# Kernel tuning notes

Hardware: AMD Instinct MI355X
Metric: run time of the kernel (lower is better)

The kernel has to match this reference:

```python
import jax, jax.numpy as jnp
import numpy as np

B, N, S = 16, 4096, 1024
D1, D2 = 128, 256          # points1 / points2 channel dims
IN_CH, OUT_CH = D1 + D2, 128
EPS_BN = 1e-5


def setup_inputs() -> dict:
    key = jax.random.key(0)
    ks = jax.random.split(key, 16)
    inp = {
        "xyz1": jax.random.normal(ks[0], (B, N, 3), jnp.float32),
        "xyz2": jax.random.normal(ks[1], (B, S, 3), jnp.float32),
        "points1": jax.random.normal(ks[2], (B, D1, N), jnp.float32),
        "points2": jax.random.normal(ks[3], (B, D2, S), jnp.float32),
        # fuse: 1x1 Conv (IN_CH -> OUT_CH) + BN + ReLU
        "fuse_w": jax.random.normal(ks[4], (OUT_CH, IN_CH), jnp.float32) * 0.05,
        "fuse_b": jnp.zeros((OUT_CH,), jnp.float32),
        "fuse_g": jnp.ones((OUT_CH,), jnp.float32),
        "fuse_be": jnp.zeros((OUT_CH,), jnp.float32),
        # extraction: 1 residual pointwise block (res_expansion=1.0)
        "w1": jax.random.normal(ks[5], (OUT_CH, OUT_CH), jnp.float32) * 0.05,
        "b1": jnp.zeros((OUT_CH,), jnp.float32),
        "g1": jnp.ones((OUT_CH,), jnp.float32),
        "be1": jnp.zeros((OUT_CH,), jnp.float32),
        "w2": jax.random.normal(ks[6], (OUT_CH, OUT_CH), jnp.float32) * 0.05,
        "b2": jnp.zeros((OUT_CH,), jnp.float32),
        "g2": jnp.ones((OUT_CH,), jnp.float32),
        "be2": jnp.zeros((OUT_CH,), jnp.float32),
    }
    return inp


def _bn(x, gamma, beta):
    # train-mode batchnorm over (batch, point) dims; x: [B, N, C]
    mu = jnp.mean(x, axis=(0, 1), keepdims=True)
    var = jnp.var(x, axis=(0, 1), keepdims=True)
    return (x - mu) * jax.lax.rsqrt(var + EPS_BN) * gamma + beta


def reference(xyz1, xyz2, points1, points2,
              fuse_w, fuse_b, fuse_g, fuse_be,
              w1, b1, g1, be1, w2, b2, g2, be2):
    # points2 -> [B, S, D2]
    p2 = jnp.transpose(points2, (0, 2, 1))
    # squared pairwise distances [B, N, S]
    d = (jnp.sum(xyz1 * xyz1, -1)[:, :, None]
         + jnp.sum(xyz2 * xyz2, -1)[:, None, :]
         - 2.0 * jnp.einsum("bnc,bsc->bns", xyz1, xyz2))
    # 3 nearest neighbors (equiv to full sort + [:, :, :3])
    neg_d3, idx = jax.lax.top_k(-d, 3)          # [B, N, 3]
    d3 = -neg_d3
    recip = 1.0 / (d3 + 1e-8)
    weight = recip / jnp.sum(recip, axis=2, keepdims=True)  # [B, N, 3]
    gathered = p2[jnp.arange(B)[:, None, None], idx]        # [B, N, 3, D2]
    interp = jnp.sum(gathered * weight[..., None], axis=2)  # [B, N, D2]
    # concat skip features: [B, N, D1+D2]
    feats = jnp.concatenate([jnp.transpose(points1, (0, 2, 1)), interp], axis=-1)
    # fuse: 1x1 conv + BN + ReLU
    x = jnp.einsum("bnc,oc->bno", feats, fuse_w) + fuse_b
    x = jax.nn.relu(_bn(x, fuse_g, fuse_be))
    # extraction: residual pointwise block
    h = jnp.einsum("bnc,oc->bno", x, w1) + b1
    h = jax.nn.relu(_bn(h, g1, be1))
    h = jnp.einsum("bnc,oc->bno", h, w2) + b2
    h = _bn(h, g2, be2)
    out = jax.nn.relu(h + x)
    return jnp.transpose(out, (0, 2, 1))  # [B, OUT_CH, N]
```

## Files before the change

### kernel.cpp

```cpp
#include <hip/hip_runtime.h>

#define BB   16
#define NN   4096
#define SS   1024
#define D1C  128
#define D2C  256
#define CIN  384
#define CO   128
#define MM   (BB*NN)

typedef __attribute__((ext_vector_type(8))) short short8;
typedef __attribute__((ext_vector_type(8))) unsigned short ushort8;
typedef __attribute__((ext_vector_type(4))) float f32x4;

__device__ __forceinline__ unsigned short f2bf(float f) {
  unsigned u = __builtin_bit_cast(unsigned, f);
  u += 0x7fffu + ((u >> 16) & 1u);
  return (unsigned short)(u >> 16);
}
__device__ __forceinline__ float bf2f(unsigned short u) {
  unsigned x = ((unsigned)u) << 16;
  return __builtin_bit_cast(float, x);
}
__device__ __forceinline__ unsigned cvt_pk(float lo, float hi) {
  unsigned r;
  asm("v_cvt_pk_bf16_f32 %0, %1, %2" : "=v"(r) : "v"(lo), "v"(hi));
  return r;
}
__device__ __forceinline__ ushort8 ld8(const unsigned short* p) {
  return *(const ushort8*)p;
}

__global__ __launch_bounds__(64) void arrange_all(
    const float* __restrict__ w0, const float* __restrict__ w1, const float* __restrict__ w2,
    uint4* __restrict__ wf0, uint4* __restrict__ wf1, uint4* __restrict__ wf2) {
  int blk = blockIdx.x;
  const float* w; uint4* wf; int K; int local;
  if (blk < 96)       { w = w0; wf = wf0; K = CIN; local = blk; }
  else if (blk < 128) { w = w1; wf = wf1; K = CO;  local = blk - 96; }
  else                { w = w2; wf = wf2; K = CO;  local = blk - 128; }
  int lane = threadIdx.x;
  int id = local * 64 + lane;
  int ob = (id >> 6) & 7;
  int kt = id >> 9;
  int o = ob * 16 + (lane & 15);
  int k = kt * 32 + (lane >> 4) * 8;
  const float* src = w + (size_t)o * K + k;
  union { unsigned short u[8]; uint4 v; } p;
  #pragma unroll
  for (int j = 0; j < 8; ++j) p.u[j] = f2bf(src[j]);
  wf[id] = p.v;
}

__global__ __launch_bounds__(256) void transp2(const float* __restrict__ p2,
                                               unsigned short* __restrict__ p2t) {
  int b  = blockIdx.x >> 6;
  int s0 = (blockIdx.x & 63) * 16;
  int c  = threadIdx.x;
  const float* src = p2 + ((size_t)b * D2C + c) * SS + s0;
  float v[16];
  #pragma unroll
  for (int k = 0; k < 4; ++k) {
    float4 x = *(const float4*)(src + k * 4);
    v[k*4+0] = x.x; v[k*4+1] = x.y; v[k*4+2] = x.z; v[k*4+3] = x.w;
  }
  unsigned short* dst = p2t + ((size_t)b * SS + s0) * D2C + c;
  #pragma unroll
  for (int s = 0; s < 16; ++s) dst[(size_t)s * D2C] = f2bf(v[s]);
}

__global__ __launch_bounds__(256) void transp1(const float* __restrict__ p1,
                                               unsigned short* __restrict__ p1t) {
  int b  = blockIdx.x >> 7;
  int n0 = (blockIdx.x & 127) * 32;
  int c  = threadIdx.x & 127;
  int nh = threadIdx.x >> 7;
  int n  = n0 + nh * 16;
  const float* src = p1 + ((size_t)b * D1C + c) * NN + n;
  float v[16];
  #pragma unroll
  for (int k = 0; k < 4; ++k) {
    float4 x = *(const float4*)(src + k * 4);
    v[k*4+0] = x.x; v[k*4+1] = x.y; v[k*4+2] = x.z; v[k*4+3] = x.w;
  }
  unsigned short* dst = p1t + ((size_t)b * NN + n) * D1C + c;
  #pragma unroll
  for (int s = 0; s < 16; ++s) dst[(size_t)s * D1C] = f2bf(v[s]);
}

#define INS(dd, ii) { if ((dd) < d2) { if ((dd) < d1) { if ((dd) < d0) { \
  d2=d1;i2=i1; d1=d0;i1=i0; d0=(dd);i0=(ii); } else { d2=d1;i2=i1; d1=(dd);i1=(ii); } } \
  else { d2=(dd);i2=(ii); } } }

__global__ __launch_bounds__(256) void top3_kernel(const float* __restrict__ xyz1,
                                                   const float* __restrict__ xyz2,
                                                   int* __restrict__ idx3,
                                                   float* __restrict__ w3) {
  __shared__ float4 sp[8 * 129 - 1];
  int b  = blockIdx.x >> 7;
  int nb = (blockIdx.x & 127) * 32;
  int t  = threadIdx.x;
  const float* x2 = xyz2 + (size_t)b * SS * 3;
  for (int i = t; i < SS; i += 256) {
    float a = x2[i*3+0], c = x2[i*3+1], d = x2[i*3+2];
    sp[(i >> 7) * 129 + (i & 127)] = make_float4(-2.f*a, -2.f*c, -2.f*d, a*a + c*c + d*d);
  }
  __syncthreads();
  int nl = t >> 3, q = t & 7;
  int n  = nb + nl;
  size_t gm = (size_t)b * NN + n;
  float px = xyz1[gm*3+0], py = xyz1[gm*3+1], pz = xyz1[gm*3+2];
  float d0 = 3.4e38f, d1 = 3.4e38f, d2 = 3.4e38f;
  int   i0 = 0, i1 = 0, i2 = 0;
  const float4* myq = sp + q * 129;
  int ibase = q * 128;
  #pragma unroll 4
  for (int s = 0; s < 128; ++s) {
    float4 p = myq[s];
    float d = fmaf(px, p.x, fmaf(py, p.y, fmaf(pz, p.z, p.w)));
    int i = ibase + s;
    bool c0 = d < d0, c1 = d < d1, c2 = d < d2;
    i2 = c2 ? (c1 ? i1 : i) : i2;
    i1 = c1 ? (c0 ? i0 : i) : i1;
    i0 = c0 ? i : i0;
    d2 = __builtin_amdgcn_fmed3f(d1, d2, d);
    d1 = __builtin_amdgcn_fmed3f(d0, d1, d);
    d0 = fminf(d0, d);
  }
  #pragma unroll
  for (int msk = 1; msk <= 4; msk <<= 1) {
    float e0 = __shfl_xor(d0, msk), e1 = __shfl_xor(d1, msk), e2 = __shfl_xor(d2, msk);
    int   j0 = __shfl_xor(i0, msk), j1 = __shfl_xor(i1, msk), j2 = __shfl_xor(i2, msk);
    INS(e0, j0); INS(e1, j1); INS(e2, j2);
  }
  if (q == 0) {
    float n1 = px*px + py*py + pz*pz;
    float r0 = 1.0f/(d0 + n1 + 1e-8f), r1 = 1.0f/(d1 + n1 + 1e-8f), r2 = 1.0f/(d2 + n1 + 1e-8f);
    float inv = 1.0f/(r0 + r1 + r2);
    idx3[gm*3+0] = i0; idx3[gm*3+1] = i1; idx3[gm*3+2] = i2;
    w3  [gm*3+0] = r0*inv; w3[gm*3+1] = r1*inv; w3[gm*3+2] = r2*inv;
  }
}

__device__ __forceinline__ void gemm_epilogue(
    f32x4 acc[8], const float* __restrict__ bias,
    unsigned short* __restrict__ outb, float* __restrict__ pblk,
    int m0b, int wid, int cl, int g, int t, int rawblk) {
  __shared__ unsigned short tile[64][136];
  __shared__ float sS[256], sQ[256];
  #pragma unroll
  for (int ob = 0; ob < 8; ++ob) {
    float4 bs = *(const float4*)(bias + ob * 16 + g * 4);
    float v0 = acc[ob][0] + bs.x, v1 = acc[ob][1] + bs.y;
    float v2 = acc[ob][2] + bs.z, v3 = acc[ob][3] + bs.w;
    uint2 pk;
    pk.x = cvt_pk(v0, v1);
    pk.y = cvt_pk(v2, v3);
    *(uint2*)&tile[wid * 16 + cl][ob * 16 + g * 4] = pk;
  }
  __syncthreads();
  int c = t & 127, half = t >> 7;
  float s = 0.f, q = 0.f;
  #pragma unroll
  for (int i = 0; i < 32; ++i) {
    float v = bf2f(tile[half * 32 + i][c]);
    s += v; q = fmaf(v, v, q);
  }
  sS[t] = s; sQ[t] = q;
  int m_l = t >> 2, cq = (t & 3) * 32;
  unsigned short* gdst = outb + (size_t)(m0b + m_l) * CO + cq;
  #pragma unroll
  for (int qd = 0; qd < 4; ++qd)
    *(uint4*)(gdst + qd * 8) = *(const uint4*)&tile[m_l][cq + qd * 8];
  __syncthreads();
  if (t < 128) {
    pblk[(size_t)rawblk * 256 + t]       = sS[t] + sS[t + 128];
    pblk[(size_t)rawblk * 256 + 128 + t] = sQ[t] + sQ[t + 128];
  }
}

__global__ __launch_bounds__(256, 4) void gemm1_mfma(
    const unsigned short* __restrict__ p1t, const unsigned short* __restrict__ p2t,
    const int* __restrict__ idx3, const float* __restrict__ w3,
    const uint4* __restrict__ wfrag, const float* __restrict__ bias,
    unsigned short* __restrict__ outb, float* __restrict__ pblk) {
  int t = threadIdx.x;
  int wid = t >> 6, lane = t & 63;
  int rawblk = blockIdx.x;
  int bid = (rawblk & 7) * 128 + (rawblk >> 3);
  int m0b = bid * 64;
  int m0 = m0b + wid * 16;
  int b  = m0 >> 12;
  int cl = lane & 15, g = lane >> 4;
  int m  = m0 + cl;
  int i0 = idx3[(size_t)m*3+0], i1 = idx3[(size_t)m*3+1], i2 = idx3[(size_t)m*3+2];
  float wA = w3[(size_t)m*3+0], wB = w3[(size_t)m*3+1], wC = w3[(size_t)m*3+2];
  const unsigned short* r0 = p2t + ((size_t)b * SS + i0) * D2C + g * 8;
  const unsigned short* r1 = p2t + ((size_t)b * SS + i1) * D2C + g * 8;
  const unsigned short* r2 = p2t + ((size_t)b * SS + i2) * D2C + g * 8;
  const unsigned short* pr = p1t + (size_t)m * D1C + g * 8;

  ushort8 pt[4], ua[4][3];
  #pragma unroll
  for (int kt = 0; kt < 4; ++kt) pt[kt] = ld8(pr + kt * 32);
  #pragma unroll
  for (int q = 0; q < 4; ++q) {
    int c0 = q * 32;
    ua[q][0] = ld8(r0 + c0); ua[q][1] = ld8(r1 + c0); ua[q][2] = ld8(r2 + c0);
  }
  f32x4 acc[8] = {};
  #pragma unroll
  for (int kt = 0; kt < 4; ++kt) {
    short8 bv = __builtin_bit_cast(short8, pt[kt]);
    const uint4* wk = wfrag + (size_t)kt * 512 + lane;
    #pragma unroll
    for (int ob = 0; ob < 8; ++ob)
      acc[ob] = __builtin_amdgcn_mfma_f32_16x16x32_bf16(
          __builtin_bit_cast(short8, wk[ob * 64]), bv, acc[ob], 0, 0, 0);
  }
  #pragma unroll
  for (int q = 0; q < 4; ++q) {
    float f[8];
    #pragma unroll
    for (int j = 0; j < 8; ++j)
      f[j] = wA*bf2f(ua[q][0][j]) + wB*bf2f(ua[q][1][j]) + wC*bf2f(ua[q][2][j]);
    uint4 pk;
    pk.x = cvt_pk(f[0], f[1]); pk.y = cvt_pk(f[2], f[3]);
    pk.z = cvt_pk(f[4], f[5]); pk.w = cvt_pk(f[6], f[7]);
    short8 bv = __builtin_bit_cast(short8, pk);
    const uint4* wk = wfrag + (size_t)(4 + q) * 512 + lane;
    #pragma unroll
    for (int ob = 0; ob < 8; ++ob)
      acc[ob] = __builtin_amdgcn_mfma_f32_16x16x32_bf16(
          __builtin_bit_cast(short8, wk[ob * 64]), bv, acc[ob], 0, 0, 0);
  }
  __builtin_amdgcn_sched_barrier(0);
  ushort8 ub[4][3];
  #pragma unroll
  for (int q = 0; q < 4; ++q) {
    int c0 = 128 + q * 32;
    ub[q][0] = ld8(r0 + c0); ub[q][1] = ld8(r1 + c0); ub[q][2] = ld8(r2 + c0);
  }
  #pragma unroll
  for (int q = 0; q < 4; ++q) {
    float f[8];
    #pragma unroll
    for (int j = 0; j < 8; ++j)
      f[j] = wA*bf2f(ub[q][0][j]) + wB*bf2f(ub[q][1][j]) + wC*bf2f(ub[q][2][j]);
    uint4 pk;
    pk.x = cvt_pk(f[0], f[1]); pk.y = cvt_pk(f[2], f[3]);
    pk.z = cvt_pk(f[4], f[5]); pk.w = cvt_pk(f[6], f[7]);
    short8 bv = __builtin_bit_cast(short8, pk);
    const uint4* wk = wfrag + (size_t)(8 + q) * 512 + lane;
    #pragma unroll
    for (int ob = 0; ob < 8; ++ob)
      acc[ob] = __builtin_amdgcn_mfma_f32_16x16x32_bf16(
          __builtin_bit_cast(short8, wk[ob * 64]), bv, acc[ob], 0, 0, 0);
  }
  gemm_epilogue(acc, bias, outb, pblk, m0b, wid, cl, g, t, rawblk);
}

__global__ __launch_bounds__(256, 4) void gemm23_mfma(
    const unsigned short* __restrict__ inb, const float* __restrict__ scale,
    const float* __restrict__ shift, const uint4* __restrict__ wfrag,
    const float* __restrict__ bias, unsigned short* __restrict__ outb,
    float* __restrict__ pblk) {
  int t = threadIdx.x;
  int wid = t >> 6, lane = t & 63;
  int rawblk = blockIdx.x;
  int bid = (rawblk & 7) * 128 + (rawblk >> 3);
  int m0b = bid * 64;
  int m0 = m0b + wid * 16;
  int cl = lane & 15, g = lane >> 4;
  int m  = m0 + cl;
  const unsigned short* src = inb + (size_t)m * CO + g * 8;
  ushort8 xv[4];
  #pragma unroll
  for (int kt = 0; kt < 4; ++kt) xv[kt] = ld8(src + kt * 32);
  f32x4 acc[8] = {};
  #pragma unroll
  for (int kt = 0; kt < 4; ++kt) {
    int kb = kt * 32 + g * 8;
    float4 sa = *(const float4*)(scale + kb), sb = *(const float4*)(scale + kb + 4);
    float4 ha = *(const float4*)(shift + kb), hb = *(const float4*)(shift + kb + 4);
    float f[8];
    f[0] = fmaxf(fmaf(bf2f(xv[kt][0]), sa.x, ha.x), 0.f);
    f[1] = fmaxf(fmaf(bf2f(xv[kt][1]), sa.y, ha.y), 0.f);
    f[2] = fmaxf(fmaf(bf2f(xv[kt][2]), sa.z, ha.z), 0.f);
    f[3] = fmaxf(fmaf(bf2f(xv[kt][3]), sa.w, ha.w), 0.f);
    f[4] = fmaxf(fmaf(bf2f(xv[kt][4]), sb.x, hb.x), 0.f);
    f[5] = fmaxf(fmaf(bf2f(xv[kt][5]), sb.y, hb.y), 0.f);
    f[6] = fmaxf(fmaf(bf2f(xv[kt][6]), sb.z, hb.z), 0.f);
    f[7] = fmaxf(fmaf(bf2f(xv[kt][7]), sb.w, hb.w), 0.f);
    uint4 pk;
    pk.x = cvt_pk(f[0], f[1]); pk.y = cvt_pk(f[2], f[3]);
    pk.z = cvt_pk(f[4], f[5]); pk.w = cvt_pk(f[6], f[7]);
    short8 bv = __builtin_bit_cast(short8, pk);
    const uint4* wk = wfrag + (size_t)kt * 512 + lane;
    #pragma unroll
    for (int ob = 0; ob < 8; ++ob)
      acc[ob] = __builtin_amdgcn_mfma_f32_16x16x32_bf16(
          __builtin_bit_cast(short8, wk[ob * 64]), bv, acc[ob], 0, 0, 0);
  }
  gemm_epilogue(acc, bias, outb, pblk, m0b, wid, cl, g, t, rawblk);
}

__global__ __launch_bounds__(256) void reduce_fin(const float* __restrict__ pblk,
                                                  const float* __restrict__ g,
                                                  const float* __restrict__ be,
                                                  float* __restrict__ scale,
                                                  float* __restrict__ shift) {
  int o = blockIdx.x, t = threadIdx.x;
  float s = 0.f, q = 0.f;
  #pragma unroll
  for (int it = 0; it < 4; ++it) {
    const float* p = pblk + (size_t)(it * 256 + t) * 256;
    s += p[o]; q += p[128 + o];
  }
  #pragma unroll
  for (int off = 32; off; off >>= 1) { s += __shfl_down(s, off, 64); q += __shfl_down(q, off, 64); }
  __shared__ float ls[4], lq[4];
  if ((t & 63) == 0) { ls[t >> 6] = s; lq[t >> 6] = q; }
  __syncthreads();
  if (t == 0) {
    float S = ls[0]+ls[1]+ls[2]+ls[3], Q = lq[0]+lq[1]+lq[2]+lq[3];
    const float invM = 1.0f / (float)MM;
    float mean = S * invM;
    float var  = Q * invM - mean * mean;
    float rstd = rsqrtf(var + 1e-5f);
    float sc   = g[o] * rstd;
    scale[o] = sc;
    shift[o] = fmaf(-mean, sc, be[o]);
  }
}

__global__ __launch_bounds__(256) void final_kernel(
    const unsigned short* __restrict__ bufX, const unsigned short* __restrict__ bufH2,
    const float* __restrict__ bnp, float* __restrict__ out) {
  __shared__ float yt[128][33];
  __shared__ float sb[512];
  int t = threadIdx.x;
  if (t < 128) {
    sb[t]       = bnp[t];
    sb[128 + t] = bnp[128 + t];
    sb[256 + t] = bnp[512 + t];
    sb[384 + t] = bnp[640 + t];
  }
  __syncthreads();
  int m0 = blockIdx.x * 32;
  int b  = m0 >> 12;
  int n0 = m0 & (NN - 1);
  int m_l = t >> 3;
  int cq  = (t & 7) * 16;
  size_t base = (size_t)(m0 + m_l) * CO + cq;
  ushort8 xu0 = ld8(bufX  + base), xu1 = ld8(bufX  + base + 8);
  ushort8 hu0 = ld8(bufH2 + base), hu1 = ld8(bufH2 + base + 8);
  #pragma unroll
  for (int j = 0; j < 16; ++j) {
    int c = cq + j;
    float x = bf2f(j < 8 ? xu0[j & 7] : xu1[j & 7]);
    float h = bf2f(j < 8 ? hu0[j & 7] : hu1[j & 7]);
    float y = fmaxf(fmaf(h, sb[256 + c], sb[384 + c]) +
                    fmaxf(fmaf(x, sb[c], sb[128 + c]), 0.f), 0.f);
    yt[c][m_l] = y;
  }
  __syncthreads();
  int o  = t >> 1;
  int nh = (t & 1) * 16;
  float* dst = out + (size_t)b * CO * NN + (size_t)o * NN + n0 + nh;
  #pragma unroll
  for (int qd = 0; qd < 4; ++qd)
    *(float4*)(dst + qd * 4) = make_float4(yt[o][nh + qd*4 + 0], yt[o][nh + qd*4 + 1],
                                           yt[o][nh + qd*4 + 2], yt[o][nh + qd*4 + 3]);
}

extern "C" void kernel_launch(void* const* d_in, const int* in_sizes, int n_in,
                              void* d_out, int out_size, void* d_ws, size_t ws_size,
                              hipStream_t stream) {
  const float* xyz1    = (const float*)d_in[0];
  const float* xyz2    = (const float*)d_in[1];
  const float* points1 = (const float*)d_in[2];
  const float* points2 = (const float*)d_in[3];
  const float* fuse_w  = (const float*)d_in[4];
  const float* fuse_b  = (const float*)d_in[5];
  const float* fuse_g  = (const float*)d_in[6];
  const float* fuse_be = (const float*)d_in[7];
  const float* w1      = (const float*)d_in[8];
  const float* b1      = (const float*)d_in[9];
  const float* g1      = (const float*)d_in[10];
  const float* be1     = (const float*)d_in[11];
  const float* w2      = (const float*)d_in[12];
  const float* b2      = (const float*)d_in[13];
  const float* g2      = (const float*)d_in[14];
  const float* be2     = (const float*)d_in[15];

  char* ws = (char*)d_ws;
  size_t off = 0;
  auto alloc = [&](size_t bytes) -> void* {
    void* p = ws + off;
    off += (bytes + 255) & ~(size_t)255;
    return p;
  };
  int*            idx3 = (int*)           alloc((size_t)MM * 3 * 4);
  float*          w3   = (float*)         alloc((size_t)MM * 3 * 4);
  uint4*          wf0  = (uint4*)         alloc((size_t)96 * 64 * 16);
  uint4*          wf1  = (uint4*)         alloc((size_t)32 * 64 * 16);
  uint4*          wf2  = (uint4*)         alloc((size_t)32 * 64 * 16);
  float*          pblk = (float*)         alloc((size_t)1024 * 256 * 4);
  float*          bnp  = (float*)         alloc(6 * 128 * 4);
  unsigned short* p2t  = (unsigned short*)alloc((size_t)BB * SS * D2C * 2);
  unsigned short* p1t  = (unsigned short*)alloc((size_t)MM * D1C * 2);
  unsigned short* bufX = (unsigned short*)alloc((size_t)MM * CO * 2);
  unsigned short* bufH = (unsigned short*)alloc((size_t)MM * CO * 2);
  unsigned short* bufH2= (unsigned short*)alloc((size_t)MM * CO * 2);
  if (off > ws_size) return;

  arrange_all<<<160, 64, 0, stream>>>(fuse_w, w1, w2, wf0, wf1, wf2);
  transp2<<<BB * 64, 256, 0, stream>>>(points2, p2t);
  transp1<<<BB * 128, 256, 0, stream>>>(points1, p1t);
  top3_kernel<<<MM/32, 256, 0, stream>>>(xyz1, xyz2, idx3, w3);

  gemm1_mfma<<<MM/64, 256, 0, stream>>>(p1t, p2t, idx3, w3, wf0, fuse_b, bufX, pblk);
  reduce_fin<<<128, 256, 0, stream>>>(pblk, fuse_g, fuse_be, bnp + 0, bnp + 128);

  gemm23_mfma<<<MM/64, 256, 0, stream>>>(bufX, bnp + 0, bnp + 128, wf1, b1, bufH, pblk);
  reduce_fin<<<128, 256, 0, stream>>>(pblk, g1, be1, bnp + 256, bnp + 384);

  gemm23_mfma<<<MM/64, 256, 0, stream>>>(bufH, bnp + 256, bnp + 384, wf2, b2, bufH2, pblk);
  reduce_fin<<<128, 256, 0, stream>>>(pblk, g2, be2, bnp + 512, bnp + 640);

  final_kernel<<<MM/32, 256, 0, stream>>>(bufX, bufH2, bnp, (float*)d_out);
}
```

Before: 263.9 us.

## Merge preprocessing kernels and fold BN stat reduction into GEMM epilogues

```diff
diff --git a/kernel.cpp b/kernel.cpp
--- a/kernel.cpp
+++ b/kernel.cpp
@@ -31,131 +31,137 @@
   return *(const ushort8*)p;
 }
 
-__global__ __launch_bounds__(64) void arrange_all(
-    const float* __restrict__ w0, const float* __restrict__ w1, const float* __restrict__ w2,
-    uint4* __restrict__ wf0, uint4* __restrict__ wf1, uint4* __restrict__ wf2) {
-  int blk = blockIdx.x;
-  const float* w; uint4* wf; int K; int local;
-  if (blk < 96)       { w = w0; wf = wf0; K = CIN; local = blk; }
-  else if (blk < 128) { w = w1; wf = wf1; K = CO;  local = blk - 96; }
-  else                { w = w2; wf = wf2; K = CO;  local = blk - 128; }
-  int lane = threadIdx.x;
-  int id = local * 64 + lane;
-  int ob = (id >> 6) & 7;
-  int kt = id >> 9;
-  int o = ob * 16 + (lane & 15);
-  int k = kt * 32 + (lane >> 4) * 8;
-  const float* src = w + (size_t)o * K + k;
-  union { unsigned short u[8]; uint4 v; } p;
-  #pragma unroll
-  for (int j = 0; j < 8; ++j) p.u[j] = f2bf(src[j]);
-  wf[id] = p.v;
-}
-
-__global__ __launch_bounds__(256) void transp2(const float* __restrict__ p2,
-                                               unsigned short* __restrict__ p2t) {
-  int b  = blockIdx.x >> 6;
-  int s0 = (blockIdx.x & 63) * 16;
-  int c  = threadIdx.x;
-  const float* src = p2 + ((size_t)b * D2C + c) * SS + s0;
-  float v[16];
-  #pragma unroll
-  for (int k = 0; k < 4; ++k) {
-    float4 x = *(const float4*)(src + k * 4);
-    v[k*4+0] = x.x; v[k*4+1] = x.y; v[k*4+2] = x.z; v[k*4+3] = x.w;
-  }
-  unsigned short* dst = p2t + ((size_t)b * SS + s0) * D2C + c;
-  #pragma unroll
-  for (int s = 0; s < 16; ++s) dst[(size_t)s * D2C] = f2bf(v[s]);
-}
-
-__global__ __launch_bounds__(256) void transp1(const float* __restrict__ p1,
-                                               unsigned short* __restrict__ p1t) {
-  int b  = blockIdx.x >> 7;
-  int n0 = (blockIdx.x & 127) * 32;
-  int c  = threadIdx.x & 127;
-  int nh = threadIdx.x >> 7;
-  int n  = n0 + nh * 16;
-  const float* src = p1 + ((size_t)b * D1C + c) * NN + n;
-  float v[16];
-  #pragma unroll
-  for (int k = 0; k < 4; ++k) {
-    float4 x = *(const float4*)(src + k * 4);
-    v[k*4+0] = x.x; v[k*4+1] = x.y; v[k*4+2] = x.z; v[k*4+3] = x.w;
-  }
-  unsigned short* dst = p1t + ((size_t)b * NN + n) * D1C + c;
-  #pragma unroll
-  for (int s = 0; s < 16; ++s) dst[(size_t)s * D1C] = f2bf(v[s]);
-}
-
 #define INS(dd, ii) { if ((dd) < d2) { if ((dd) < d1) { if ((dd) < d0) { \
   d2=d1;i2=i1; d1=d0;i1=i0; d0=(dd);i0=(ii); } else { d2=d1;i2=i1; d1=(dd);i1=(ii); } } \
   else { d2=(dd);i2=(ii); } } }
 
-__global__ __launch_bounds__(256) void top3_kernel(const float* __restrict__ xyz1,
-                                                   const float* __restrict__ xyz2,
-                                                   int* __restrict__ idx3,
-                                                   float* __restrict__ w3) {
-  __shared__ float4 sp[8 * 129 - 1];
-  int b  = blockIdx.x >> 7;
-  int nb = (blockIdx.x & 127) * 32;
-  int t  = threadIdx.x;
-  const float* x2 = xyz2 + (size_t)b * SS * 3;
-  for (int i = t; i < SS; i += 256) {
-    float a = x2[i*3+0], c = x2[i*3+1], d = x2[i*3+2];
-    sp[(i >> 7) * 129 + (i & 127)] = make_float4(-2.f*a, -2.f*c, -2.f*d, a*a + c*c + d*d);
-  }
-  __syncthreads();
-  int nl = t >> 3, q = t & 7;
-  int n  = nb + nl;
-  size_t gm = (size_t)b * NN + n;
-  float px = xyz1[gm*3+0], py = xyz1[gm*3+1], pz = xyz1[gm*3+2];
-  float d0 = 3.4e38f, d1 = 3.4e38f, d2 = 3.4e38f;
-  int   i0 = 0, i1 = 0, i2 = 0;
-  const float4* myq = sp + q * 129;
-  int ibase = q * 128;
-  #pragma unroll 4
-  for (int s = 0; s < 128; ++s) {
-    float4 p = myq[s];
-    float d = fmaf(px, p.x, fmaf(py, p.y, fmaf(pz, p.z, p.w)));
-    int i = ibase + s;
-    bool c0 = d < d0, c1 = d < d1, c2 = d < d2;
-    i2 = c2 ? (c1 ? i1 : i) : i2;
-    i1 = c1 ? (c0 ? i0 : i) : i1;
-    i0 = c0 ? i : i0;
-    d2 = __builtin_amdgcn_fmed3f(d1, d2, d);
-    d1 = __builtin_amdgcn_fmed3f(d0, d1, d);
-    d0 = fminf(d0, d);
-  }
-  #pragma unroll
-  for (int msk = 1; msk <= 4; msk <<= 1) {
-    float e0 = __shfl_xor(d0, msk), e1 = __shfl_xor(d1, msk), e2 = __shfl_xor(d2, msk);
-    int   j0 = __shfl_xor(i0, msk), j1 = __shfl_xor(i1, msk), j2 = __shfl_xor(i2, msk);
-    INS(e0, j0); INS(e1, j1); INS(e2, j2);
-  }
-  if (q == 0) {
-    float n1 = px*px + py*py + pz*pz;
-    float r0 = 1.0f/(d0 + n1 + 1e-8f), r1 = 1.0f/(d1 + n1 + 1e-8f), r2 = 1.0f/(d2 + n1 + 1e-8f);
-    float inv = 1.0f/(r0 + r1 + r2);
-    idx3[gm*3+0] = i0; idx3[gm*3+1] = i1; idx3[gm*3+2] = i2;
-    w3  [gm*3+0] = r0*inv; w3[gm*3+1] = r1*inv; w3[gm*3+2] = r2*inv;
+__global__ __launch_bounds__(256) void prep_kernel(
+    const float* __restrict__ xyz1, const float* __restrict__ xyz2,
+    const float* __restrict__ p1, const float* __restrict__ p2,
+    const float* __restrict__ fw, const float* __restrict__ w1, const float* __restrict__ w2,
+    int* __restrict__ idx3, float* __restrict__ w3,
+    uint4* __restrict__ wf0, uint4* __restrict__ wf1, uint4* __restrict__ wf2,
+    unsigned short* __restrict__ p2t, unsigned short* __restrict__ p1t,
+    float* __restrict__ zeroRegion) {
+  __shared__ float4 sp[1032];
+  int blk = blockIdx.x, t = threadIdx.x;
+  if (blk == 0) {
+    for (int i = t; i < 832; i += 256) zeroRegion[i] = 0.f;
+  }
+  {
+    int u = blk * 2;
+    int b = u >> 7;
+    const float* x2 = xyz2 + (size_t)b * SS * 3;
+    for (int i = t; i < SS; i += 256) {
+      float a = x2[i*3+0], c = x2[i*3+1], d = x2[i*3+2];
+      sp[(i >> 7) * 129 + (i & 127)] = make_float4(-2.f*a, -2.f*c, -2.f*d, a*a + c*c + d*d);
+    }
+    __syncthreads();
+    int nl = t >> 3, q = t & 7;
+    const float4* myq = sp + q * 129;
+    int ibase = q * 128;
+    for (int uu = 0; uu < 2; ++uu) {
+      int nb = ((u + uu) & 127) * 32;
+      int n  = nb + nl;
+      size_t gm = (size_t)b * NN + n;
+      float px = xyz1[gm*3+0], py = xyz1[gm*3+1], pz = xyz1[gm*3+2];
+      float d0 = 3.4e38f, d1 = 3.4e38f, d2 = 3.4e38f;
+      int   i0 = 0, i1 = 0, i2 = 0;
+      #pragma unroll 4
+      for (int s = 0; s < 128; ++s) {
+        float4 p = myq[s];
+        float d = fmaf(px, p.x, fmaf(py, p.y, fmaf(pz, p.z, p.w)));
+        int i = ibase + s;
+        bool c0 = d < d0, c1 = d < d1, c2 = d < d2;
+        i2 = c2 ? (c1 ? i1 : i) : i2;
+        i1 = c1 ? (c0 ? i0 : i) : i1;
+        i0 = c0 ? i : i0;
+        d2 = __builtin_amdgcn_fmed3f(d1, d2, d);
+        d1 = __builtin_amdgcn_fmed3f(d0, d1, d);
+        d0 = fminf(d0, d);
+      }
+      #pragma unroll
+      for (int msk = 1; msk <= 4; msk <<= 1) {
+        float e0 = __shfl_xor(d0, msk), e1 = __shfl_xor(d1, msk), e2 = __shfl_xor(d2, msk);
+        int   j0 = __shfl_xor(i0, msk), j1 = __shfl_xor(i1, msk), j2 = __shfl_xor(i2, msk);
+        INS(e0, j0); INS(e1, j1); INS(e2, j2);
+      }
+      if (q == 0) {
+        float n1 = px*px + py*py + pz*pz;
+        float r0 = 1.0f/(d0 + n1 + 1e-8f), r1 = 1.0f/(d1 + n1 + 1e-8f), r2 = 1.0f/(d2 + n1 + 1e-8f);
+        float inv = 1.0f/(r0 + r1 + r2);
+        idx3[gm*3+0] = i0; idx3[gm*3+1] = i1; idx3[gm*3+2] = i2;
+        w3  [gm*3+0] = r0*inv; w3[gm*3+1] = r1*inv; w3[gm*3+2] = r2*inv;
+      }
+    }
+  }
+  {
+    int b  = blk >> 6;
+    int s0 = (blk & 63) * 16;
+    int c  = t;
+    const float* src = p2 + ((size_t)b * D2C + c) * SS + s0;
+    float v[16];
+    #pragma unroll
+    for (int k = 0; k < 4; ++k) {
+      float4 x = *(const float4*)(src + k * 4);
+      v[k*4+0] = x.x; v[k*4+1] = x.y; v[k*4+2] = x.z; v[k*4+3] = x.w;
+    }
+    unsigned short* dst = p2t + ((size_t)b * SS + s0) * D2C + c;
+    #pragma unroll
+    for (int s = 0; s < 16; ++s) dst[(size_t)s * D2C] = f2bf(v[s]);
+  }
+  for (int uu = 0; uu < 2; ++uu) {
+    int u  = blk * 2 + uu;
+    int b  = u >> 7;
+    int n0 = (u & 127) * 32;
+    int c  = t & 127;
+    int n  = n0 + (t >> 7) * 16;
+    const float* src = p1 + ((size_t)b * D1C + c) * NN + n;
+    float v[16];
+    #pragma unroll
+    for (int k = 0; k < 4; ++k) {
+      float4 x = *(const float4*)(src + k * 4);
+      v[k*4+0] = x.x; v[k*4+1] = x.y; v[k*4+2] = x.z; v[k*4+3] = x.w;
+    }
+    unsigned short* dst = p1t + ((size_t)b * NN + n) * D1C + c;
+    #pragma unroll
+    for (int s = 0; s < 16; ++s) dst[(size_t)s * D1C] = f2bf(v[s]);
+  }
+  if (blk < 40) {
+    int gid = blk * 256 + t;
+    int oblk = gid >> 6, lane = gid & 63;
+    const float* w; uint4* wf; int K; int local;
+    if (oblk < 96)       { w = fw; wf = wf0; K = CIN; local = oblk; }
+    else if (oblk < 128) { w = w1; wf = wf1; K = CO;  local = oblk - 96; }
+    else                 { w = w2; wf = wf2; K = CO;  local = oblk - 128; }
+    int id = local * 64 + lane;
+    int ob = (id >> 6) & 7;
+    int kt = id >> 9;
+    int o = ob * 16 + (lane & 15);
+    int k = kt * 32 + (lane >> 4) * 8;
+    const float* src = w + (size_t)o * K + k;
+    union { unsigned short us[8]; uint4 v; } pk;
+    #pragma unroll
+    for (int j = 0; j < 8; ++j) pk.us[j] = f2bf(src[j]);
+    wf[id] = pk.v;
   }
 }
 
 __device__ __forceinline__ void gemm_epilogue(
     f32x4 acc[8], const float* __restrict__ bias,
-    unsigned short* __restrict__ outb, float* __restrict__ pblk,
-    int m0b, int wid, int cl, int g, int t, int rawblk) {
+    unsigned short* __restrict__ outb, int m0b, int wid, int cl, int g, int t,
+    float* __restrict__ gsum, float* __restrict__ gssq, unsigned* __restrict__ counter,
+    const float* __restrict__ gamma, const float* __restrict__ beta,
+    float* __restrict__ scale, float* __restrict__ shift) {
   __shared__ unsigned short tile[64][136];
   __shared__ float sS[256], sQ[256];
+  __shared__ int lastFlag;
   #pragma unroll
   for (int ob = 0; ob < 8; ++ob) {
     float4 bs = *(const float4*)(bias + ob * 16 + g * 4);
-    float v0 = acc[ob][0] + bs.x, v1 = acc[ob][1] + bs.y;
-    float v2 = acc[ob][2] + bs.z, v3 = acc[ob][3] + bs.w;
     uint2 pk;
-    pk.x = cvt_pk(v0, v1);
-    pk.y = cvt_pk(v2, v3);
+    pk.x = cvt_pk(acc[ob][0] + bs.x, acc[ob][1] + bs.y);
+    pk.y = cvt_pk(acc[ob][2] + bs.z, acc[ob][3] + bs.w);
     *(uint2*)&tile[wid * 16 + cl][ob * 16 + g * 4] = pk;
   }
   __syncthreads();
@@ -174,8 +180,24 @@
     *(uint4*)(gdst + qd * 8) = *(const uint4*)&tile[m_l][cq + qd * 8];
   __syncthreads();
   if (t < 128) {
-    pblk[(size_t)rawblk * 256 + t]       = sS[t] + sS[t + 128];
-    pblk[(size_t)rawblk * 256 + 128 + t] = sQ[t] + sQ[t + 128];
+    atomicAdd(&gsum[t], sS[t] + sS[t + 128]);
+    atomicAdd(&gssq[t], sQ[t] + sQ[t + 128]);
+  }
+  __threadfence();
+  __syncthreads();
+  if (t == 0) lastFlag = (atomicAdd(counter, 1u) == 1023u);
+  __syncthreads();
+  if (lastFlag && t < 128) {
+    __threadfence();
+    float S = atomicAdd(&gsum[t], 0.f);
+    float Q = atomicAdd(&gssq[t], 0.f);
+    const float invM = 1.0f / (float)MM;
+    float mean = S * invM;
+    float var  = Q * invM - mean * mean;
+    float rstd = rsqrtf(var + 1e-5f);
+    float sc   = gamma[t] * rstd;
+    scale[t] = sc;
+    shift[t] = fmaf(-mean, sc, beta[t]);
   }
 }
 
@@ -183,7 +205,10 @@
     const unsigned short* __restrict__ p1t, const unsigned short* __restrict__ p2t,
     const int* __restrict__ idx3, const float* __restrict__ w3,
     const uint4* __restrict__ wfrag, const float* __restrict__ bias,
-    unsigned short* __restrict__ outb, float* __restrict__ pblk) {
+    unsigned short* __restrict__ outb,
+    float* __restrict__ gsum, float* __restrict__ gssq, unsigned* __restrict__ counter,
+    const float* __restrict__ gamma, const float* __restrict__ beta,
+    float* __restrict__ scale, float* __restrict__ shift) {
   int t = threadIdx.x;
   int wid = t >> 6, lane = t & 63;
   int rawblk = blockIdx.x;
@@ -199,7 +224,6 @@
   const unsigned short* r1 = p2t + ((size_t)b * SS + i1) * D2C + g * 8;
   const unsigned short* r2 = p2t + ((size_t)b * SS + i2) * D2C + g * 8;
   const unsigned short* pr = p1t + (size_t)m * D1C + g * 8;
-
   ushort8 pt[4], ua[4][3];
   #pragma unroll
   for (int kt = 0; kt < 4; ++kt) pt[kt] = ld8(pr + kt * 32);
@@ -257,14 +281,17 @@
       acc[ob] = __builtin_amdgcn_mfma_f32_16x16x32_bf16(
           __builtin_bit_cast(short8, wk[ob * 64]), bv, acc[ob], 0, 0, 0);
   }
-  gemm_epilogue(acc, bias, outb, pblk, m0b, wid, cl, g, t, rawblk);
+  gemm_epilogue(acc, bias, outb, m0b, wid, cl, g, t,
+                gsum, gssq, counter, gamma, beta, scale, shift);
 }
 
 __global__ __launch_bounds__(256, 4) void gemm23_mfma(
-    const unsigned short* __restrict__ inb, const float* __restrict__ scale,
-    const float* __restrict__ shift, const uint4* __restrict__ wfrag,
+    const unsigned short* __restrict__ inb, const float* __restrict__ scIn,
+    const float* __restrict__ shIn, const uint4* __restrict__ wfrag,
     const float* __restrict__ bias, unsigned short* __restrict__ outb,
-    float* __restrict__ pblk) {
+    float* __restrict__ gsum, float* __restrict__ gssq, unsigned* __restrict__ counter,
+    const float* __restrict__ gamma, const float* __restrict__ beta,
+    float* __restrict__ scale, float* __restrict__ shift) {
   int t = threadIdx.x;
   int wid = t >> 6, lane = t & 63;
   int rawblk = blockIdx.x;
@@ -281,8 +308,8 @@
   #pragma unroll
   for (int kt = 0; kt < 4; ++kt) {
     int kb = kt * 32 + g * 8;
-    float4 sa = *(const float4*)(scale + kb), sb = *(const float4*)(scale + kb + 4);
-    float4 ha = *(const float4*)(shift + kb), hb = *(const float4*)(shift + kb + 4);
+    float4 sa = *(const float4*)(scIn + kb), sb = *(const float4*)(scIn + kb + 4);
+    float4 ha = *(const float4*)(shIn + kb), hb = *(const float4*)(shIn + kb + 4);
     float f[8];
     f[0] = fmaxf(fmaf(bf2f(xv[kt][0]), sa.x, ha.x), 0.f);
     f[1] = fmaxf(fmaf(bf2f(xv[kt][1]), sa.y, ha.y), 0.f);
@@ -302,36 +329,8 @@
       acc[ob] = __builtin_amdgcn_mfma_f32_16x16x32_bf16(
           __builtin_bit_cast(short8, wk[ob * 64]), bv, acc[ob], 0, 0, 0);
   }
-  gemm_epilogue(acc, bias, outb, pblk, m0b, wid, cl, g, t, rawblk);
-}
-
-__global__ __launch_bounds__(256) void reduce_fin(const float* __restrict__ pblk,
-                                                  const float* __restrict__ g,
-                                                  const float* __restrict__ be,
-                                                  float* __restrict__ scale,
-                                                  float* __restrict__ shift) {
-  int o = blockIdx.x, t = threadIdx.x;
-  float s = 0.f, q = 0.f;
-  #pragma unroll
-  for (int it = 0; it < 4; ++it) {
-    const float* p = pblk + (size_t)(it * 256 + t) * 256;
-    s += p[o]; q += p[128 + o];
-  }
-  #pragma unroll
-  for (int off = 32; off; off >>= 1) { s += __shfl_down(s, off, 64); q += __shfl_down(q, off, 64); }
-  __shared__ float ls[4], lq[4];
-  if ((t & 63) == 0) { ls[t >> 6] = s; lq[t >> 6] = q; }
-  __syncthreads();
-  if (t == 0) {
-    float S = ls[0]+ls[1]+ls[2]+ls[3], Q = lq[0]+lq[1]+lq[2]+lq[3];
-    const float invM = 1.0f / (float)MM;
-    float mean = S * invM;
-    float var  = Q * invM - mean * mean;
-    float rstd = rsqrtf(var + 1e-5f);
-    float sc   = g[o] * rstd;
-    scale[o] = sc;
-    shift[o] = fmaf(-mean, sc, be[o]);
-  }
+  gemm_epilogue(acc, bias, outb, m0b, wid, cl, g, t,
+                gsum, gssq, counter, gamma, beta, scale, shift);
 }
 
 __global__ __launch_bounds__(256) void final_kernel(
@@ -360,9 +359,8 @@
     int c = cq + j;
     float x = bf2f(j < 8 ? xu0[j & 7] : xu1[j & 7]);
     float h = bf2f(j < 8 ? hu0[j & 7] : hu1[j & 7]);
-    float y = fmaxf(fmaf(h, sb[256 + c], sb[384 + c]) +
-                    fmaxf(fmaf(x, sb[c], sb[128 + c]), 0.f), 0.f);
-    yt[c][m_l] = y;
+    yt[c][m_l] = fmaxf(fmaf(h, sb[256 + c], sb[384 + c]) +
+                       fmaxf(fmaf(x, sb[c], sb[128 + c]), 0.f), 0.f);
   }
   __syncthreads();
   int o  = t >> 1;
@@ -401,33 +399,36 @@
     off += (bytes + 255) & ~(size_t)255;
     return p;
   };
-  int*            idx3 = (int*)           alloc((size_t)MM * 3 * 4);
-  float*          w3   = (float*)         alloc((size_t)MM * 3 * 4);
-  uint4*          wf0  = (uint4*)         alloc((size_t)96 * 64 * 16);
-  uint4*          wf1  = (uint4*)         alloc((size_t)32 * 64 * 16);
-  uint4*          wf2  = (uint4*)         alloc((size_t)32 * 64 * 16);
-  float*          pblk = (float*)         alloc((size_t)1024 * 256 * 4);
-  float*          bnp  = (float*)         alloc(6 * 128 * 4);
-  unsigned short* p2t  = (unsigned short*)alloc((size_t)BB * SS * D2C * 2);
-  unsigned short* p1t  = (unsigned short*)alloc((size_t)MM * D1C * 2);
-  unsigned short* bufX = (unsigned short*)alloc((size_t)MM * CO * 2);
-  unsigned short* bufH = (unsigned short*)alloc((size_t)MM * CO * 2);
-  unsigned short* bufH2= (unsigned short*)alloc((size_t)MM * CO * 2);
+  int*            idx3  = (int*)           alloc((size_t)MM * 3 * 4);
+  float*          w3    = (float*)         alloc((size_t)MM * 3 * 4);
+  uint4*          wf0   = (uint4*)         alloc((size_t)96 * 64 * 16);
+  uint4*          wf1   = (uint4*)         alloc((size_t)32 * 64 * 16);
+  uint4*          wf2   = (uint4*)         alloc((size_t)32 * 64 * 16);
+  float*          stats = (float*)         alloc(6 * 128 * 4);
+  unsigned*       ctr   = (unsigned*)      alloc(256);
+  float*          bnp   = (float*)         alloc(6 * 128 * 4);
+  unsigned short* p2t   = (unsigned short*)alloc((size_t)BB * SS * D2C * 2);
+  unsigned short* p1t   = (unsigned short*)alloc((size_t)MM * D1C * 2);
+  unsigned short* bufX  = (unsigned short*)alloc((size_t)MM * CO * 2);
+  unsigned short* bufH  = (unsigned short*)alloc((size_t)MM * CO * 2);
+  unsigned short* bufH2 = (unsigned short*)alloc((size_t)MM * CO * 2);
   if (off > ws_size) return;
 
-  arrange_all<<<160, 64, 0, stream>>>(fuse_w, w1, w2, wf0, wf1, wf2);
-  transp2<<<BB * 64, 256, 0, stream>>>(points2, p2t);
-  transp1<<<BB * 128, 256, 0, stream>>>(points1, p1t);
-  top3_kernel<<<MM/32, 256, 0, stream>>>(xyz1, xyz2, idx3, w3);
-
-  gemm1_mfma<<<MM/64, 256, 0, stream>>>(p1t, p2t, idx3, w3, wf0, fuse_b, bufX, pblk);
-  reduce_fin<<<128, 256, 0, stream>>>(pblk, fuse_g, fuse_be, bnp + 0, bnp + 128);
-
-  gemm23_mfma<<<MM/64, 256, 0, stream>>>(bufX, bnp + 0, bnp + 128, wf1, b1, bufH, pblk);
-  reduce_fin<<<128, 256, 0, stream>>>(pblk, g1, be1, bnp + 256, bnp + 384);
-
-  gemm23_mfma<<<MM/64, 256, 0, stream>>>(bufH, bnp + 256, bnp + 384, wf2, b2, bufH2, pblk);
-  reduce_fin<<<128, 256, 0, stream>>>(pblk, g2, be2, bnp + 512, bnp + 640);
+  prep_kernel<<<1024, 256, 0, stream>>>(xyz1, xyz2, points1, points2,
+                                        fuse_w, w1, w2, idx3, w3, wf0, wf1, wf2,
+                                        p2t, p1t, stats );
+
+  gemm1_mfma<<<1024, 256, 0, stream>>>(p1t, p2t, idx3, w3, wf0, fuse_b, bufX,
+                                       stats + 0, stats + 128, ctr + 0,
+                                       fuse_g, fuse_be, bnp + 0, bnp + 128);
+
+  gemm23_mfma<<<1024, 256, 0, stream>>>(bufX, bnp + 0, bnp + 128, wf1, b1, bufH,
+                                        stats + 256, stats + 384, ctr + 1,
+                                        g1, be1, bnp + 256, bnp + 384);
+
+  gemm23_mfma<<<1024, 256, 0, stream>>>(bufH, bnp + 256, bnp + 384, wf2, b2, bufH2,
+                                        stats + 512, stats + 640, ctr + 2,
+                                        g2, be2, bnp + 512, bnp + 640);
 
   final_kernel<<<MM/32, 256, 0, stream>>>(bufX, bufH2, bnp, (float*)d_out);
 }
```

After: 668.6 us. 153% more time.
